# Performance work log

Hardware: AMD Instinct MI355X
Metric: run time of the kernel (lower is better)

## Reference

```python
import jax, jax.numpy as jnp
import numpy as np

N, D, H = 4096, 1024, 4096
EPS = 1e-5


def setup_inputs() -> dict:
    key = jax.random.key(0)
    ks = jax.random.split(key, 12)
    s_in = 1.0 / np.sqrt(D)
    s_hid = 1.0 / np.sqrt(H)
    return {
        "x": jax.random.normal(ks[0], (N, D), dtype=jnp.float32),
        "Wq": jax.random.uniform(ks[1], (D, H), jnp.float32, -s_in, s_in),
        "Wk": jax.random.uniform(ks[2], (D, H), jnp.float32, -s_in, s_in),
        "Wv": jax.random.uniform(ks[3], (D, H), jnp.float32, -s_in, s_in),
        "Wo": jax.random.uniform(ks[4], (H, D), jnp.float32, -s_hid, s_hid),
        "W1": jax.random.uniform(ks[5], (D, H), jnp.float32, -s_in, s_in),
        "b1": jax.random.uniform(ks[6], (H,), jnp.float32, -s_in, s_in),
        "W2": jax.random.uniform(ks[7], (H, D), jnp.float32, -s_hid, s_hid),
        "b2": jax.random.uniform(ks[8], (D,), jnp.float32, -s_hid, s_hid),
        "g1": jnp.ones((D,), jnp.float32),
        "be1": jnp.zeros((D,), jnp.float32),
        "g2": jnp.ones((D,), jnp.float32),
        "be2": jnp.zeros((D,), jnp.float32),
    }


def _layernorm(x, g, b):
    mu = jnp.mean(x, axis=-1, keepdims=True)
    var = jnp.mean(jnp.square(x - mu), axis=-1, keepdims=True)
    return (x - mu) * jax.lax.rsqrt(var + EPS) * g + b


def reference(x, Wq, Wk, Wv, Wo, W1, b1, W2, b2, g1, be1, g2, be2):
    # --- attention (single head, unscaled, as in the source) ---
    q = x @ Wq                      # [N, H]
    k = x @ Wk                      # [N, H]
    v = x @ Wv                      # [N, H]
    scores = jax.nn.softmax(q @ k.T, axis=-1)  # [N, N]
    attn = (scores @ v) @ Wo        # [N, D]
    h = _layernorm(x + attn, g1, be1)
    # --- feed-forward ---
    ff = jax.nn.relu(h @ W1 + b1) @ W2 + b2
    return _layernorm(h + ff, g2, be2)
```

## Files before the change

kernel.cpp:

```cpp
#include <hip/hip_runtime.h>
#include <hip/hip_bf16.h>

using f16 = _Float16;
typedef __attribute__((ext_vector_type(8))) f16 half8;
typedef __attribute__((ext_vector_type(4))) f16 half4;
typedef __attribute__((ext_vector_type(4))) float floatx4;

#define LN_EPS 1e-5f

__device__ __forceinline__ void gload_lds16(const f16* g, f16* l) {
  __builtin_amdgcn_global_load_lds(
      (const __attribute__((address_space(1))) void*)g,
      (__attribute__((address_space(3))) void*)l, 16, 0, 0);
}

#define CFENCE asm volatile("" ::: "memory")
#define WAIT_VM(N) asm volatile("s_waitcnt vmcnt(" #N ")" ::: "memory")
#define BARRIER()                    \
  do {                               \
    CFENCE;                          \
    __builtin_amdgcn_s_barrier();    \
    CFENCE;                          \
  } while (0)

template <int EPI>
__device__ __forceinline__ void gemm_core(
    const f16* __restrict__ A, const f16* __restrict__ B,
    f16* __restrict__ Ch, const float* __restrict__ bias,
    int lda, int ldb, int ldc, int kper, int kbeg, int bm, int bn,
    f16* As, f16* Bs) {
  const int t = threadIdx.x;
  const int wave = t >> 6, lane = t & 63;
  const int wm = (wave >> 1) << 6;
  const int wn = (wave & 1) << 6;
  const int lrow = lane & 15;
  const int lkc = lane >> 4;

  floatx4 acc[4][4] = {};

  const int segr = lane >> 3;
  const int segc = (lane & 7) << 3;
  const f16* Ag = A + (size_t)(bm + wave * 32 + segr) * lda + kbeg + segc;
  const f16* Bg = B + (size_t)(bn + wave * 32 + segr) * ldb + kbeg + segc;
  f16* AsW = As + wave * 4 * 512;
  f16* BsW = Bs + wave * 4 * 512;

  const f16* ApL = As + (wm + lrow) * 64 + lkc * 8;
  const f16* BpL = Bs + (wn + lrow) * 64 + lkc * 8;

  for (int kit = 0; kit < kper; kit += 64) {
#pragma unroll
    for (int l = 0; l < 4; ++l) {
      gload_lds16(Ag + (size_t)(l * 8) * lda, AsW + l * 512);
      gload_lds16(Bg + (size_t)(l * 8) * ldb, BsW + l * 512);
    }
    Ag += 64;
    Bg += 64;
    __syncthreads();
#pragma unroll
    for (int kk = 0; kk < 2; ++kk) {
      half8 af[4], bfr[4];
#pragma unroll
      for (int i = 0; i < 4; ++i)
        af[i] = *(const half8*)(ApL + kk * 32 + i * (16 * 64));
#pragma unroll
      for (int j = 0; j < 4; ++j)
        bfr[j] = *(const half8*)(BpL + kk * 32 + j * (16 * 64));
#pragma unroll
      for (int i = 0; i < 4; ++i)
#pragma unroll
        for (int j = 0; j < 4; ++j)
          acc[i][j] = __builtin_amdgcn_mfma_f32_16x16x32_f16(af[i], bfr[j],
                                                             acc[i][j], 0, 0, 0);
    }
    __syncthreads();
  }

  const int crow0 = bm + wm + lkc * 4;
  const int ccol0 = bn + wn + lrow;
#pragma unroll
  for (int i = 0; i < 4; ++i) {
#pragma unroll
    for (int r = 0; r < 4; ++r) {
      const size_t row = (size_t)(crow0 + i * 16 + r);
#pragma unroll
      for (int j = 0; j < 4; ++j) {
        const int col = ccol0 + j * 16;
        float v = acc[i][j][r];
        if (EPI == 2) v = fmaxf(v + bias[col], 0.0f);
        Ch[row * (size_t)ldc + col] = (f16)v;
      }
    }
  }
}

template <int EPI>
__global__ __launch_bounds__(512, 2) void gemm256(
    const f16* __restrict__ A, const f16* __restrict__ B,
    f16* __restrict__ Ch, const float* __restrict__ bias,
    int M, int Nc, int K, int lda, int ldb, int ldc) {
  __shared__ f16 sm[4][256 * 64];

  const int gx = gridDim.x, gy = gridDim.y;
  const int nwg = gx * gy * gridDim.z;
  const int id = blockIdx.x + gx * (blockIdx.y + gy * blockIdx.z);
  const int q = nwg >> 3, r = nwg & 7;
  const int xcd = id & 7, lin = id >> 3;
  const int nid = (xcd < r ? xcd * (q + 1) : r * (q + 1) + (xcd - r) * q) + lin;
  const int bx = nid % gx;
  const int by = (nid / gx) % gy;
  const int bz = nid / (gx * gy);

  const int kper = K / gridDim.z;
  const int kbeg = bz * kper;
  f16* Cz = Ch + (size_t)bz * M * ldc;
  const int bm = by << 8, bn = bx << 8;

  const int t = threadIdx.x;
  const int wave = t >> 6, lane = t & 63;
  const int wm = (wave >> 2) << 7;
  const int wn = (wave & 3) << 6;
  const int lrow = lane & 15, lkc = lane >> 4;

  const int srow = lane >> 3;
  const int schunk = ((lane & 7) ^ srow) << 3;
  const f16* Ag = A + (size_t)(bm + wave * 16 + srow) * lda + kbeg + schunk;
  const f16* Bg = B + (size_t)(bn + wave * 16 + srow) * ldb + kbeg + schunk;

  const int co0 = ((lkc ^ (lrow & 7)) << 3);
  const int co1 = (((4 + lkc) ^ (lrow & 7)) << 3);

  floatx4 acc[8][4] = {};
  half8 af[4][2];
  half8 bf[2][2][2];

  auto STAGE = [&](int b, int tt, int h) {
    if (h < 2) {
      const f16* src = Ag + (size_t)(h * 128) * lda + tt * 64;
      f16* d = &sm[b * 2][h * 8192 + wave * 1024];
      gload_lds16(src, d);
      gload_lds16(src + (size_t)8 * lda, d + 512);
    } else {
      const f16* src = Bg + (size_t)((h - 2) * 128) * ldb + tt * 64;
      f16* d = &sm[b * 2 + 1][(h - 2) * 8192 + wave * 1024];
      gload_lds16(src, d);
      gload_lds16(src + (size_t)8 * ldb, d + 512);
    }
  };
  auto LDA = [&](int b, int qm) {
    const f16* base = &sm[b * 2][(wm + qm * 64 + lrow) * 64];
#pragma unroll
    for (int fm = 0; fm < 4; ++fm) {
      af[fm][0] = *(const half8*)(base + fm * (16 * 64) + co0);
      af[fm][1] = *(const half8*)(base + fm * (16 * 64) + co1);
    }
  };
  auto LDB = [&](int b, int qn) {
    const f16* base = &sm[b * 2 + 1][(wn + qn * 32 + lrow) * 64];
#pragma unroll
    for (int fn = 0; fn < 2; ++fn) {
      bf[qn][fn][0] = *(const half8*)(base + fn * (16 * 64) + co0);
      bf[qn][fn][1] = *(const half8*)(base + fn * (16 * 64) + co1);
    }
  };
  auto MFMAQ = [&](int qm, int qn) {
    __builtin_amdgcn_s_setprio(1);
#pragma unroll
    for (int kk = 0; kk < 2; ++kk)
#pragma unroll
      for (int fm = 0; fm < 4; ++fm)
#pragma unroll
        for (int fn = 0; fn < 2; ++fn)
          acc[qm * 4 + fm][qn * 2 + fn] =
              __builtin_amdgcn_mfma_f32_16x16x32_f16(
                  af[fm][kk], bf[qn][fn][kk], acc[qm * 4 + fm][qn * 2 + fn],
                  0, 0, 0);
    __builtin_amdgcn_s_setprio(0);
  };

  const int NT = kper >> 6;
  const int NI = NT >> 1;

  STAGE(0, 0, 0); STAGE(0, 0, 1); STAGE(0, 0, 2); STAGE(0, 0, 3);
  STAGE(1, 1, 0);
  WAIT_VM(2);
  BARRIER();

  for (int i = 0; i < NI; ++i) {
    const bool last = (i == NI - 1);
    const int tb = 2 * i;
    LDA(0, 0); LDB(0, 0); STAGE(1, tb + 1, 1);
    BARRIER(); MFMAQ(0, 0); BARRIER();
    LDB(0, 1); STAGE(1, tb + 1, 2);
    BARRIER(); MFMAQ(0, 1); BARRIER();
    LDA(0, 1); STAGE(1, tb + 1, 3);
    BARRIER(); MFMAQ(1, 0); BARRIER();
    if (!last) {
      STAGE(0, tb + 2, 0);
      WAIT_VM(2);
    } else {
      WAIT_VM(0);
    }
    BARRIER(); MFMAQ(1, 1); BARRIER();
    LDA(1, 0); LDB(1, 0);
    if (!last) STAGE(0, tb + 2, 1);
    BARRIER(); MFMAQ(0, 0); BARRIER();
    LDB(1, 1);
    if (!last) STAGE(0, tb + 2, 2);
    BARRIER(); MFMAQ(0, 1); BARRIER();
    LDA(1, 1);
    if (!last) STAGE(0, tb + 2, 3);
    BARRIER(); MFMAQ(1, 0); BARRIER();
    if (!last) {
      STAGE(1, tb + 3, 0);
      WAIT_VM(2);
    }
    BARRIER(); MFMAQ(1, 1); BARRIER();
  }

  const int crow0 = bm + wm + lkc * 4;
  const int ccol0 = bn + wn + lrow;
#pragma unroll
  for (int i = 0; i < 8; ++i) {
#pragma unroll
    for (int r2 = 0; r2 < 4; ++r2) {
      const size_t row = (size_t)(crow0 + i * 16 + r2);
#pragma unroll
      for (int j = 0; j < 4; ++j) {
        const int col = ccol0 + j * 16;
        float v = acc[i][j][r2];
        if (EPI == 2) v = fmaxf(v + bias[col], 0.0f);
        Cz[row * (size_t)ldc + col] = (f16)v;
      }
    }
  }
}

__global__ __launch_bounds__(256) void gemm_pre(
    const f16* __restrict__ Wkb, const f16* __restrict__ Wqb,
    const f16* __restrict__ WoT, const f16* __restrict__ Wvb,
    f16* __restrict__ parQK, f16* __restrict__ parVO, int D, int H) {
  __shared__ f16 As[128 * 64];
  __shared__ f16 Bs[128 * 64];
  const int z = blockIdx.z, zz = z & 7;
  const f16* A = (z < 8) ? Wkb : WoT;
  const f16* B = (z < 8) ? Wqb : Wvb;
  f16* slab = ((z < 8) ? parQK : parVO) + (size_t)zz * D * D;
  gemm_core<1>(A, B, slab, nullptr, H, H, D, H / 8, zz * (H / 8),
               blockIdx.y << 7, blockIdx.x << 7, As, Bs);
}

__global__ __launch_bounds__(256) void gemm_dual(
    const f16* __restrict__ xb, const f16* __restrict__ WqkT,
    const f16* __restrict__ WvoT, f16* __restrict__ th,
    f16* __restrict__ xvoT, int N, int D) {
  __shared__ f16 As[128 * 64];
  __shared__ f16 Bs[128 * 64];
  const int y = blockIdx.y;
  if (y < 32)
    gemm_core<1>(xb, WqkT, th, nullptr, D, D, D, D, 0,
                 y << 7, blockIdx.x << 7, As, Bs);
  else
    gemm_core<1>(WvoT, xb, xvoT, nullptr, D, D, N, D, 0,
                 blockIdx.x << 7, (y - 32) << 7, As, Bs);
}

__global__ void prep_inputs(const float* x, const float* Wq, const float* Wk,
                            const float* Wv, const float* W1, const float* Wo,
                            const float* W2, f16* xb, f16* Wqb, f16* Wkb,
                            f16* Wvb, f16* W1T, f16* WoT, f16* W2T) {
  const int z = blockIdx.z;
  const int tx = threadIdx.x, ty = threadIdx.y;
  if (z >= 3) {
    const int t = ty * 32 + tx;
    const float* in;
    f16* out;
    size_t row, col, C;
    if (z == 3) {
      in = x; out = xb; C = 1024;
      row = blockIdx.x * 32 + (t >> 3);
      col = blockIdx.y * 32 + (t & 7) * 4;
    } else {
      in = (z == 4) ? Wq : (z == 5) ? Wk : Wv;
      out = (z == 4) ? Wqb : (z == 5) ? Wkb : Wvb;
      C = 4096;
      row = blockIdx.y * 32 + (t >> 3);
      col = blockIdx.x * 32 + (t & 7) * 4;
    }
    const float4 f = *(const float4*)(in + row * C + col);
    f16* o = out + row * C + col;
    o[0] = (f16)f.x; o[1] = (f16)f.y; o[2] = (f16)f.z; o[3] = (f16)f.w;
    return;
  }
  const float* in;
  f16* out;
  int R, C, r0, c0;
  if (z == 0) {
    R = 1024; C = 4096;
    r0 = blockIdx.y * 32; c0 = blockIdx.x * 32;
    in = W1; out = W1T;
  } else {
    R = 4096; C = 1024;
    r0 = blockIdx.x * 32; c0 = blockIdx.y * 32;
    in = (z == 1) ? Wo : W2;
    out = (z == 1) ? WoT : W2T;
  }
  __shared__ float tile[32][33];
#pragma unroll
  for (int i = 0; i < 32; i += 8)
    tile[ty + i][tx] = in[(size_t)(r0 + ty + i) * C + (c0 + tx)];
  __syncthreads();
#pragma unroll
  for (int i = 0; i < 32; i += 8)
    out[(size_t)(c0 + ty + i) * R + (r0 + tx)] = (f16)tile[tx][ty + i];
}

__global__ void reduce_dual(const f16* __restrict__ parQK,
                            const f16* __restrict__ parVO,
                            f16* __restrict__ WqkT, f16* __restrict__ WvoT,
                            int n) {
  const int half = gridDim.x >> 1;
  const bool second = blockIdx.x >= half;
  const f16* par = second ? parVO : parQK;
  f16* out = second ? WvoT : WqkT;
  const int b = second ? blockIdx.x - half : blockIdx.x;
  const int i = (b * 256 + threadIdx.x) * 4;
  float s0 = 0, s1 = 0, s2 = 0, s3 = 0;
#pragma unroll
  for (int z = 0; z < 8; ++z) {
    const half4 p = *(const half4*)(par + (size_t)z * n + i);
    s0 += (float)p[0]; s1 += (float)p[1]; s2 += (float)p[2]; s3 += (float)p[3];
  }
  half4 o = {(f16)s0, (f16)s1, (f16)s2, (f16)s3};
  *(half4*)(out + i) = o;
}

__global__ void softmax_rows(const f16* __restrict__ S, f16* __restrict__ P,
                             int N) {
  const int row = blockIdx.x;
  const int t = threadIdx.x;
  const int lane = t & 63, wave = t >> 6;
  const f16* s = S + (size_t)row * N;
  const half8 a = *(const half8*)(s + t * 8);
  const half8 b = *(const half8*)(s + 2048 + t * 8);
  float v[16];
#pragma unroll
  for (int i = 0; i < 8; ++i) {
    v[i] = (float)a[i];
    v[8 + i] = (float)b[i];
  }
  float mx = -1e30f;
#pragma unroll
  for (int i = 0; i < 16; ++i) mx = fmaxf(mx, v[i]);
#pragma unroll
  for (int off = 32; off > 0; off >>= 1) mx = fmaxf(mx, __shfl_xor(mx, off));
  __shared__ float red[8];
  if (lane == 0) red[wave] = mx;
  __syncthreads();
  mx = fmaxf(fmaxf(red[0], red[1]), fmaxf(red[2], red[3]));
  float sum = 0.0f;
#pragma unroll
  for (int i = 0; i < 16; ++i) {
    v[i] = __expf(v[i] - mx);
    sum += v[i];
  }
#pragma unroll
  for (int off = 32; off > 0; off >>= 1) sum += __shfl_xor(sum, off);
  if (lane == 0) red[4 + wave] = sum;
  __syncthreads();
  const float inv = 1.0f / (red[4] + red[5] + red[6] + red[7]);
  f16* p = P + (size_t)row * N;
  half8 oa, ob;
#pragma unroll
  for (int i = 0; i < 8; ++i) {
    oa[i] = (f16)(v[i] * inv);
    ob[i] = (f16)(v[8 + i] * inv);
  }
  *(half8*)(p + t * 8) = oa;
  *(half8*)(p + 2048 + t * 8) = ob;
}

__global__ void add_ln(const float* __restrict__ a, const f16* __restrict__ b,
                       int nchunks, size_t cs, const float* __restrict__ bias,
                       const float* __restrict__ g, const float* __restrict__ be,
                       float* __restrict__ outf, f16* __restrict__ outh, int D) {
  const int row = blockIdx.x;
  const int t = threadIdx.x;
  const int lane = t & 63, wave = t >> 6;
  const float4 av = *(const float4*)(a + (size_t)row * D + t * 4);
  float s[4] = {av.x, av.y, av.z, av.w};
  for (int c = 0; c < nchunks; ++c) {
    const half4 bv = *(const half4*)(b + c * cs + (size_t)row * D + t * 4);
    s[0] += (float)bv[0]; s[1] += (float)bv[1];
    s[2] += (float)bv[2]; s[3] += (float)bv[3];
  }
  if (bias != nullptr) {
    const float4 bb = *(const float4*)(bias + t * 4);
    s[0] += bb.x; s[1] += bb.y; s[2] += bb.z; s[3] += bb.w;
  }
  float sum = s[0] + s[1] + s[2] + s[3];
  float sq = s[0] * s[0] + s[1] * s[1] + s[2] * s[2] + s[3] * s[3];
#pragma unroll
  for (int off = 32; off > 0; off >>= 1) {
    sum += __shfl_xor(sum, off);
    sq += __shfl_xor(sq, off);
  }
  __shared__ float red[8];
  if (lane == 0) {
    red[wave] = sum;
    red[4 + wave] = sq;
  }
  __syncthreads();
  sum = red[0] + red[1] + red[2] + red[3];
  sq = red[4] + red[5] + red[6] + red[7];
  const float mu = sum / (float)D;
  const float rv = rsqrtf(sq / (float)D - mu * mu + LN_EPS);
  const float4 gv = *(const float4*)(g + t * 4);
  const float4 bev = *(const float4*)(be + t * 4);
  float y0 = (s[0] - mu) * rv * gv.x + bev.x;
  float y1 = (s[1] - mu) * rv * gv.y + bev.y;
  float y2 = (s[2] - mu) * rv * gv.z + bev.z;
  float y3 = (s[3] - mu) * rv * gv.w + bev.w;
  if (outf != nullptr) {
    float4 o = {y0, y1, y2, y3};
    *(float4*)(outf + (size_t)row * D + t * 4) = o;
  }
  if (outh != nullptr) {
    f16* ob = outh + (size_t)row * D + t * 4;
    ob[0] = (f16)y0;
    ob[1] = (f16)y1;
    ob[2] = (f16)y2;
    ob[3] = (f16)y3;
  }
}

extern "C" void kernel_launch(void* const* d_in, const int* in_sizes, int n_in,
                              void* d_out, int out_size, void* d_ws,
                              size_t ws_size, hipStream_t stream) {
  constexpr int N = 4096, D = 1024, H = 4096;
  const float* x = (const float*)d_in[0];
  const float* Wq = (const float*)d_in[1];
  const float* Wk = (const float*)d_in[2];
  const float* Wv = (const float*)d_in[3];
  const float* Wo = (const float*)d_in[4];
  const float* W1 = (const float*)d_in[5];
  const float* b1 = (const float*)d_in[6];
  const float* W2 = (const float*)d_in[7];
  const float* b2 = (const float*)d_in[8];
  const float* g1 = (const float*)d_in[9];
  const float* be1 = (const float*)d_in[10];
  const float* g2 = (const float*)d_in[11];
  const float* be2 = (const float*)d_in[12];
  float* out = (float*)d_out;

  const size_t MB = 1024ull * 1024ull;
  char* w = (char*)d_ws;
  f16* xb   = (f16*)(w + 0 * MB);
  f16* Wqb  = (f16*)(w + 8 * MB);
  f16* Wkb  = (f16*)(w + 16 * MB);
  f16* Wvb  = (f16*)(w + 24 * MB);
  f16* WoT  = (f16*)(w + 32 * MB);
  f16* W1T  = (f16*)(w + 40 * MB);
  f16* W2T  = (f16*)(w + 48 * MB);
  f16* WqkT = (f16*)(w + 56 * MB);
  f16* WvoT = (f16*)(w + 58 * MB);
  f16* th   = (f16*)(w + 60 * MB);
  f16* xvoT = (f16*)(w + 68 * MB);
  f16* F1   = (f16*)(w + 76 * MB);
  f16* Sh   = (f16*)(w + 108 * MB);
  f16* parA = (f16*)(w + 108 * MB);
  f16* Pb   = (f16*)(w + 140 * MB);
  float* hf = (float*)(w + 172 * MB);
  f16* hb   = (f16*)(w + 188 * MB);
  f16* parQK = (f16*)(w + 196 * MB);
  f16* parVO = (f16*)(w + 212 * MB);

  prep_inputs<<<dim3(128, 32, 7), dim3(32, 8), 0, stream>>>(
      x, Wq, Wk, Wv, W1, Wo, W2, xb, Wqb, Wkb, Wvb, W1T, WoT, W2T);

  gemm_pre<<<dim3(D / 128, D / 128, 16), 256, 0, stream>>>(
      Wkb, Wqb, WoT, Wvb, parQK, parVO, D, H);
  reduce_dual<<<2 * (D * D) / 1024, 256, 0, stream>>>(parQK, parVO, WqkT,
                                                      WvoT, D * D);

  gemm_dual<<<dim3(8, 64), 256, 0, stream>>>(xb, WqkT, WvoT, th, xvoT, N, D);
  gemm256<1><<<dim3(N / 256, N / 256, 1), 512, 0, stream>>>(
      th, xb, Sh, nullptr, N, N, D, D, D, N);
  softmax_rows<<<N, 256, 0, stream>>>(Sh, Pb, N);
  gemm256<1><<<dim3(D / 256, N / 256, 4), 512, 0, stream>>>(
      Pb, xvoT, parA, nullptr, N, D, N, N, N, D);
  add_ln<<<N, 256, 0, stream>>>(x, parA, 4, (size_t)N * D, nullptr, g1, be1,
                                hf, hb, D);

  gemm256<2><<<dim3(H / 256, N / 256, 1), 512, 0, stream>>>(
      hb, W1T, F1, b1, N, H, D, D, D, H);
  gemm256<1><<<dim3(D / 256, N / 256, 4), 512, 0, stream>>>(
      F1, W2T, parA, nullptr, N, D, H, H, H, D);
  add_ln<<<N, 256, 0, stream>>>(hf, parA, 4, (size_t)N * D, b2, g2, be2,
                                out, nullptr, D);
}
```

Baseline: 431.5 us.

## Use 256x256 pipelined GEMM core for weight-product GEMMs and vectorize prep

Refactors the 256-tile pipelined GEMM into a reusable core and moves the weight-product (Wk·Wq, Wo·Wv) and dual projection GEMMs from the simple 128-tile kernel onto it, with XCD-aware block swizzling. The input prep kernel is also rewritten to do 8-wide vectorized fp16 conversion and 64x64 swizzled LDS transposes. The aim is higher MFMA efficiency and fewer memory transactions in the preprocessing GEMMs. In exchange these small GEMMs now launch far fewer workgroups (256 and 128), which may leave CUs idle.

Result: faster. 406.2 us (-5.9%).

```diff
diff --git a/kernel.cpp b/kernel.cpp
--- a/kernel.cpp
+++ b/kernel.cpp
@@ -24,98 +24,11 @@
   } while (0)
 
 template <int EPI>
-__device__ __forceinline__ void gemm_core(
+__device__ __forceinline__ void gemm256_core(
     const f16* __restrict__ A, const f16* __restrict__ B,
-    f16* __restrict__ Ch, const float* __restrict__ bias,
+    f16* __restrict__ Cz, const float* __restrict__ bias,
     int lda, int ldb, int ldc, int kper, int kbeg, int bm, int bn,
-    f16* As, f16* Bs) {
-  const int t = threadIdx.x;
-  const int wave = t >> 6, lane = t & 63;
-  const int wm = (wave >> 1) << 6;
-  const int wn = (wave & 1) << 6;
-  const int lrow = lane & 15;
-  const int lkc = lane >> 4;
-
-  floatx4 acc[4][4] = {};
-
-  const int segr = lane >> 3;
-  const int segc = (lane & 7) << 3;
-  const f16* Ag = A + (size_t)(bm + wave * 32 + segr) * lda + kbeg + segc;
-  const f16* Bg = B + (size_t)(bn + wave * 32 + segr) * ldb + kbeg + segc;
-  f16* AsW = As + wave * 4 * 512;
-  f16* BsW = Bs + wave * 4 * 512;
-
-  const f16* ApL = As + (wm + lrow) * 64 + lkc * 8;
-  const f16* BpL = Bs + (wn + lrow) * 64 + lkc * 8;
-
-  for (int kit = 0; kit < kper; kit += 64) {
-#pragma unroll
-    for (int l = 0; l < 4; ++l) {
-      gload_lds16(Ag + (size_t)(l * 8) * lda, AsW + l * 512);
-      gload_lds16(Bg + (size_t)(l * 8) * ldb, BsW + l * 512);
-    }
-    Ag += 64;
-    Bg += 64;
-    __syncthreads();
-#pragma unroll
-    for (int kk = 0; kk < 2; ++kk) {
-      half8 af[4], bfr[4];
-#pragma unroll
-      for (int i = 0; i < 4; ++i)
-        af[i] = *(const half8*)(ApL + kk * 32 + i * (16 * 64));
-#pragma unroll
-      for (int j = 0; j < 4; ++j)
-        bfr[j] = *(const half8*)(BpL + kk * 32 + j * (16 * 64));
-#pragma unroll
-      for (int i = 0; i < 4; ++i)
-#pragma unroll
-        for (int j = 0; j < 4; ++j)
-          acc[i][j] = __builtin_amdgcn_mfma_f32_16x16x32_f16(af[i], bfr[j],
-                                                             acc[i][j], 0, 0, 0);
-    }
-    __syncthreads();
-  }
-
-  const int crow0 = bm + wm + lkc * 4;
-  const int ccol0 = bn + wn + lrow;
-#pragma unroll
-  for (int i = 0; i < 4; ++i) {
-#pragma unroll
-    for (int r = 0; r < 4; ++r) {
-      const size_t row = (size_t)(crow0 + i * 16 + r);
-#pragma unroll
-      for (int j = 0; j < 4; ++j) {
-        const int col = ccol0 + j * 16;
-        float v = acc[i][j][r];
-        if (EPI == 2) v = fmaxf(v + bias[col], 0.0f);
-        Ch[row * (size_t)ldc + col] = (f16)v;
-      }
-    }
-  }
-}
-
-template <int EPI>
-__global__ __launch_bounds__(512, 2) void gemm256(
-    const f16* __restrict__ A, const f16* __restrict__ B,
-    f16* __restrict__ Ch, const float* __restrict__ bias,
-    int M, int Nc, int K, int lda, int ldb, int ldc) {
-  __shared__ f16 sm[4][256 * 64];
-
-  const int gx = gridDim.x, gy = gridDim.y;
-  const int nwg = gx * gy * gridDim.z;
-  const int id = blockIdx.x + gx * (blockIdx.y + gy * blockIdx.z);
-  const int q = nwg >> 3, r = nwg & 7;
-  const int xcd = id & 7, lin = id >> 3;
-  const int nid = (xcd < r ? xcd * (q + 1) : r * (q + 1) + (xcd - r) * q) + lin;
-  const int bx = nid % gx;
-  const int by = (nid / gx) % gy;
-  const int bz = nid / (gx * gy);
-
-  const int kper = K / gridDim.z;
-  const int kbeg = bz * kper;
-  f16* Cz = Ch + (size_t)bz * M * ldc;
-  const int bm = by << 8, bn = bx << 8;
-
+    f16* smp) {
   const int t = threadIdx.x;
   const int wave = t >> 6, lane = t & 63;
   const int wm = (wave >> 2) << 7;
@@ -137,18 +50,18 @@
   auto STAGE = [&](int b, int tt, int h) {
     if (h < 2) {
       const f16* src = Ag + (size_t)(h * 128) * lda + tt * 64;
-      f16* d = &sm[b * 2][h * 8192 + wave * 1024];
+      f16* d = smp + (b * 2) * 16384 + h * 8192 + wave * 1024;
       gload_lds16(src, d);
       gload_lds16(src + (size_t)8 * lda, d + 512);
     } else {
       const f16* src = Bg + (size_t)((h - 2) * 128) * ldb + tt * 64;
-      f16* d = &sm[b * 2 + 1][(h - 2) * 8192 + wave * 1024];
+      f16* d = smp + (b * 2 + 1) * 16384 + (h - 2) * 8192 + wave * 1024;
       gload_lds16(src, d);
       gload_lds16(src + (size_t)8 * ldb, d + 512);
     }
   };
   auto LDA = [&](int b, int qm) {
-    const f16* base = &sm[b * 2][(wm + qm * 64 + lrow) * 64];
+    const f16* base = smp + (b * 2) * 16384 + (wm + qm * 64 + lrow) * 64;
 #pragma unroll
     for (int fm = 0; fm < 4; ++fm) {
       af[fm][0] = *(const half8*)(base + fm * (16 * 64) + co0);
@@ -156,7 +69,7 @@
     }
   };
   auto LDB = [&](int b, int qn) {
-    const f16* base = &sm[b * 2 + 1][(wn + qn * 32 + lrow) * 64];
+    const f16* base = smp + (b * 2 + 1) * 16384 + (wn + qn * 32 + lrow) * 64;
 #pragma unroll
     for (int fn = 0; fn < 2; ++fn) {
       bf[qn][fn][0] = *(const half8*)(base + fn * (16 * 64) + co0);
@@ -236,83 +149,114 @@
   }
 }
 
-__global__ __launch_bounds__(256) void gemm_pre(
+__device__ __forceinline__ int xcd_swizzle(int id, int nwg) {
+  const int q = nwg >> 3, r = nwg & 7;
+  const int xcd = id & 7, lin = id >> 3;
+  return (xcd < r ? xcd * (q + 1) : r * (q + 1) + (xcd - r) * q) + lin;
+}
+
+template <int EPI>
+__global__ __launch_bounds__(512, 2) void gemm_nt256(
+    const f16* __restrict__ A, const f16* __restrict__ B,
+    f16* __restrict__ Ch, const float* __restrict__ bias,
+    int M, int Nc, int K, int lda, int ldb, int ldc) {
+  __shared__ f16 sm[4][256 * 64];
+  const int gx = gridDim.x, gy = gridDim.y;
+  const int nwg = gx * gy * gridDim.z;
+  const int id = blockIdx.x + gx * (blockIdx.y + gy * blockIdx.z);
+  const int nid = xcd_swizzle(id, nwg);
+  const int bx = nid % gx;
+  const int by = (nid / gx) % gy;
+  const int bz = nid / (gx * gy);
+  const int kper = K / gridDim.z;
+  gemm256_core<EPI>(A, B, Ch + (size_t)bz * M * ldc, bias, lda, ldb, ldc,
+                    kper, bz * kper, by << 8, bx << 8, &sm[0][0]);
+}
+
+__global__ __launch_bounds__(512, 2) void gemm_pre256(
     const f16* __restrict__ Wkb, const f16* __restrict__ Wqb,
     const f16* __restrict__ WoT, const f16* __restrict__ Wvb,
     f16* __restrict__ parQK, f16* __restrict__ parVO, int D, int H) {
-  __shared__ f16 As[128 * 64];
-  __shared__ f16 Bs[128 * 64];
-  const int z = blockIdx.z, zz = z & 7;
+  __shared__ f16 sm[4][256 * 64];
+  const int id = blockIdx.x + 4 * (blockIdx.y + 4 * blockIdx.z);
+  const int nid = xcd_swizzle(id, 256);
+  const int bx = nid & 3, by = (nid >> 2) & 3, z = nid >> 4;
+  const int zz = z & 7;
   const f16* A = (z < 8) ? Wkb : WoT;
   const f16* B = (z < 8) ? Wqb : Wvb;
   f16* slab = ((z < 8) ? parQK : parVO) + (size_t)zz * D * D;
-  gemm_core<1>(A, B, slab, nullptr, H, H, D, H / 8, zz * (H / 8),
-               blockIdx.y << 7, blockIdx.x << 7, As, Bs);
-}
-
-__global__ __launch_bounds__(256) void gemm_dual(
+  gemm256_core<1>(A, B, slab, nullptr, H, H, D, H / 8, zz * (H / 8),
+                  by << 8, bx << 8, &sm[0][0]);
+}
+
+__global__ __launch_bounds__(512, 2) void gemm_dual256(
     const f16* __restrict__ xb, const f16* __restrict__ WqkT,
     const f16* __restrict__ WvoT, f16* __restrict__ th,
     f16* __restrict__ xvoT, int N, int D) {
-  __shared__ f16 As[128 * 64];
-  __shared__ f16 Bs[128 * 64];
-  const int y = blockIdx.y;
-  if (y < 32)
-    gemm_core<1>(xb, WqkT, th, nullptr, D, D, D, D, 0,
-                 y << 7, blockIdx.x << 7, As, Bs);
+  __shared__ f16 sm[4][256 * 64];
+  const int id = blockIdx.x + 4 * blockIdx.y;
+  const int nid = xcd_swizzle(id, 128);
+  const int bx = nid & 3, y = nid >> 2;
+  if (y < 16)
+    gemm256_core<1>(xb, WqkT, th, nullptr, D, D, D, D, 0,
+                    y << 8, bx << 8, &sm[0][0]);
   else
-    gemm_core<1>(WvoT, xb, xvoT, nullptr, D, D, N, D, 0,
-                 blockIdx.x << 7, (y - 32) << 7, As, Bs);
+    gemm256_core<1>(WvoT, xb, xvoT, nullptr, D, D, N, D, 0,
+                    bx << 8, (y - 16) << 8, &sm[0][0]);
 }
 
 __global__ void prep_inputs(const float* x, const float* Wq, const float* Wk,
                             const float* Wv, const float* W1, const float* Wo,
                             const float* W2, f16* xb, f16* Wqb, f16* Wkb,
                             f16* Wvb, f16* W1T, f16* WoT, f16* W2T) {
-  const int z = blockIdx.z;
-  const int tx = threadIdx.x, ty = threadIdx.y;
+  const int z = blockIdx.y;
+  const int b = blockIdx.x;
+  const int t = threadIdx.x;
   if (z >= 3) {
-    const int t = ty * 32 + tx;
-    const float* in;
-    f16* out;
-    size_t row, col, C;
-    if (z == 3) {
-      in = x; out = xb; C = 1024;
-      row = blockIdx.x * 32 + (t >> 3);
-      col = blockIdx.y * 32 + (t & 7) * 4;
-    } else {
-      in = (z == 4) ? Wq : (z == 5) ? Wk : Wv;
-      out = (z == 4) ? Wqb : (z == 5) ? Wkb : Wvb;
-      C = 4096;
-      row = blockIdx.y * 32 + (t >> 3);
-      col = blockIdx.x * 32 + (t & 7) * 4;
-    }
-    const float4 f = *(const float4*)(in + row * C + col);
-    f16* o = out + row * C + col;
-    o[0] = (f16)f.x; o[1] = (f16)f.y; o[2] = (f16)f.z; o[3] = (f16)f.w;
+    const float* in = (z == 3) ? x : (z == 4) ? Wq : (z == 5) ? Wk : Wv;
+    f16* out = (z == 3) ? xb : (z == 4) ? Wqb : (z == 5) ? Wkb : Wvb;
+    const size_t i = ((size_t)b * 256 + t) * 8;
+    const float4 a = *(const float4*)(in + i);
+    const float4 c = *(const float4*)(in + i + 4);
+    half8 v = {(f16)a.x, (f16)a.y, (f16)a.z, (f16)a.w,
+               (f16)c.x, (f16)c.y, (f16)c.z, (f16)c.w};
+    *(half8*)(out + i) = v;
     return;
   }
+  if (b >= 1024) return;
+  int R, C, tx, ty;
   const float* in;
   f16* out;
-  int R, C, r0, c0;
   if (z == 0) {
-    R = 1024; C = 4096;
-    r0 = blockIdx.y * 32; c0 = blockIdx.x * 32;
-    in = W1; out = W1T;
+    R = 1024; C = 4096; in = W1; out = W1T;
+    tx = b & 63; ty = b >> 6;
   } else {
-    R = 4096; C = 1024;
-    r0 = blockIdx.x * 32; c0 = blockIdx.y * 32;
-    in = (z == 1) ? Wo : W2;
+    R = 4096; C = 1024; in = (z == 1) ? Wo : W2;
     out = (z == 1) ? WoT : W2T;
-  }
-  __shared__ float tile[32][33];
-#pragma unroll
-  for (int i = 0; i < 32; i += 8)
-    tile[ty + i][tx] = in[(size_t)(r0 + ty + i) * C + (c0 + tx)];
+    tx = b & 15; ty = b >> 4;
+  }
+  const int r0 = ty << 6, c0 = tx << 6;
+  __shared__ f16 lt[64 * 64];
+  const int lr = t >> 4, lc = t & 15;
+#pragma unroll
+  for (int rr = 0; rr < 4; ++rr) {
+    const int r = lr + rr * 16;
+    const float4 f = *(const float4*)(in + (size_t)(r0 + r) * C + c0 + lc * 4);
+    const float fv[4] = {f.x, f.y, f.z, f.w};
+#pragma unroll
+    for (int j = 0; j < 4; ++j) {
+      const int c = lc * 4 + j;
+      lt[c * 64 + (r ^ ((c & 7) << 3))] = (f16)fv[j];
+    }
+  }
   __syncthreads();
-#pragma unroll
-  for (int i = 0; i < 32; i += 8)
-    out[(size_t)(c0 + ty + i) * R + (r0 + tx)] = (f16)tile[tx][ty + i];
+  const int oc = t >> 3, orr = (t & 7) << 3;
+#pragma unroll
+  for (int cc = 0; cc < 2; ++cc) {
+    const int c = oc + cc * 32;
+    const half8 v = *(const half8*)(lt + c * 64 + (orr ^ ((c & 7) << 3)));
+    *(half8*)(out + (size_t)(c0 + c) * R + r0 + orr) = v;
+  }
 }
 
 __global__ void reduce_dual(const f16* __restrict__ parQK,
@@ -475,26 +419,27 @@
   f16* parQK = (f16*)(w + 196 * MB);
   f16* parVO = (f16*)(w + 212 * MB);
 
-  prep_inputs<<<dim3(128, 32, 7), dim3(32, 8), 0, stream>>>(
+  prep_inputs<<<dim3(2048, 7), 256, 0, stream>>>(
       x, Wq, Wk, Wv, W1, Wo, W2, xb, Wqb, Wkb, Wvb, W1T, WoT, W2T);
 
-  gemm_pre<<<dim3(D / 128, D / 128, 16), 256, 0, stream>>>(
+  gemm_pre256<<<dim3(4, 4, 16), 512, 0, stream>>>(
       Wkb, Wqb, WoT, Wvb, parQK, parVO, D, H);
   reduce_dual<<<2 * (D * D) / 1024, 256, 0, stream>>>(parQK, parVO, WqkT,
                                                       WvoT, D * D);
 
-  gemm_dual<<<dim3(8, 64), 256, 0, stream>>>(xb, WqkT, WvoT, th, xvoT, N, D);
-  gemm256<1><<<dim3(N / 256, N / 256, 1), 512, 0, stream>>>(
+  gemm_dual256<<<dim3(4, 32), 512, 0, stream>>>(xb, WqkT, WvoT, th, xvoT,
+                                                N, D);
+  gemm_nt256<1><<<dim3(N / 256, N / 256, 1), 512, 0, stream>>>(
       th, xb, Sh, nullptr, N, N, D, D, D, N);
   softmax_rows<<<N, 256, 0, stream>>>(Sh, Pb, N);
-  gemm256<1><<<dim3(D / 256, N / 256, 4), 512, 0, stream>>>(
+  gemm_nt256<1><<<dim3(D / 256, N / 256, 4), 512, 0, stream>>>(
       Pb, xvoT, parA, nullptr, N, D, N, N, N, D);
   add_ln<<<N, 256, 0, stream>>>(x, parA, 4, (size_t)N * D, nullptr, g1, be1,
                                 hf, hb, D);
 
-  gemm256<2><<<dim3(H / 256, N / 256, 1), 512, 0, stream>>>(
+  gemm_nt256<2><<<dim3(H / 256, N / 256, 1), 512, 0, stream>>>(
       hb, W1T, F1, b1, N, H, D, D, D, H);
-  gemm256<1><<<dim3(D / 256, N / 256, 4), 512, 0, stream>>>(
+  gemm_nt256<1><<<dim3(D / 256, N / 256, 4), 512, 0, stream>>>(
       F1, W2T, parA, nullptr, N, D, H, H, H, D);
   add_ln<<<N, 256, 0, stream>>>(hf, parA, 4, (size_t)N * D, b2, g2, be2,
                                 out, nullptr, D);
```
